# Kernel optimization log

Measured on AMD Instinct MI355X. Metric: run time of the kernel, lower is better.

The kernel has to match this reference:

```python
import jax, jax.numpy as jnp
import numpy as np

H = 28; W = 28; N = H * W
P = N              # padded max persistence pairs per homology dimension
T = 32             # landscape resolution
K1, K2 = 2, 3      # K_max for the two topo layers
M0_1, M0_2 = 0.05, 0.2
LIMS = ((1.0, 28.0), (1.0, 28.0))


def _make_nbrs(h, w, conn8):
    idx = np.arange(h * w).reshape(h, w)
    offs = [(-1, 0), (1, 0), (0, -1), (0, 1)]
    if conn8:
        offs += [(-1, -1), (-1, 1), (1, -1), (1, 1)]
    nbrs = []
    for i in range(h):
        for j in range(w):
            cur = [idx[i + a, j + b] for a, b in offs if 0 <= i + a < h and 0 <= j + b < w]
            nbrs.append(np.asarray(cur, np.int64))
    return nbrs

_NBR4 = _make_nbrs(H, W, False)
_NBR8 = _make_nbrs(H, W, True)


def _h0_pairs(vals, nbrs):
    # 0-dim persistence pairs of a vertex-valued sublevel filtration (union-find, elder rule)
    order = np.argsort(vals, kind="stable")
    pos = np.empty(N, np.int64); pos[order] = np.arange(N)
    parent = np.arange(N); birth = np.arange(N)
    added = np.zeros(N, bool)
    bi = np.zeros(P, np.int32); di = np.zeros(P, np.int32)
    k = 0
    def find(x):
        r = x
        while parent[r] != r: r = parent[r]
        while parent[x] != r: parent[x], x = r, parent[x]
        return r
    for v in order:
        added[v] = True
        for u in nbrs[v]:
            if not added[u]: continue
            ru, rv = find(u), find(v)
            if ru == rv: continue
            if pos[birth[ru]] <= pos[birth[rv]]:
                lb = birth[rv]; parent[rv] = ru
            else:
                lb = birth[ru]; parent[ru] = rv
            if k < P:
                bi[k] = lb; di[k] = v; k += 1
    return bi, di


def _pers_pairs_np(x):
    # x: [M, N] -> (birth_idx, death_idx) each [M, 2, P]; padded pairs point at idx 0 (zero persistence)
    x = np.asarray(x, np.float64)
    M = x.shape[0]
    bi = np.zeros((M, 2, P), np.int32); di = np.zeros((M, 2, P), np.int32)
    for m in range(M):
        b0, d0 = _h0_pairs(x[m], _NBR4)      # H0: sublevel, 4-connectivity
        b1, d1 = _h0_pairs(-x[m], _NBR8)     # H1 by Alexander duality: H0 of superlevel, 8-connectivity
        bi[m, 0], di[m, 0] = b0, d0
        bi[m, 1], di[m, 1] = d1, b1          # H1 birth = vals[d1], death = vals[b1]
    return bi, di


def _grid_d2():
    xs = np.linspace(LIMS[0][0], LIMS[0][1], H)
    ys = np.linspace(LIMS[1][0], LIMS[1][1], W)
    gx, gy = np.meshgrid(xs, ys, indexing="ij")
    pts = np.stack([gx.ravel(), gy.ravel()], 1)              # [N, 2] grid coordinates
    d2 = ((pts[:, None, :] - pts[None, :, :]) ** 2).sum(-1)  # [N, N] squared distances
    si = np.argsort(d2, axis=1, kind="stable")
    return jnp.asarray(si), jnp.asarray(np.take_along_axis(d2, si, 1), jnp.float32)

_SORT_IDX, _D2S = _grid_d2()


def dtm(x_flat, m0):
    # weighted distance-to-measure on the pixel grid, r=2; x_flat: [M, N] positive weights
    bound = m0 * jnp.sum(x_flat, -1, keepdims=True)                        # [M, 1]
    ws = x_flat[:, _SORT_IDX]                                              # [M, N, N] weights in distance order
    cum = jnp.cumsum(ws, -1)
    eff = jnp.minimum(jnp.maximum(bound[..., None] - (cum - ws), 0.0), ws) # effective mass per neighbor
    return jnp.sqrt(jnp.sum(eff * _D2S, -1) / bound)                       # [M, N]


def _landscape(vals, bi, di, start, end, K):
    # persistence landscape lambda_k sampled on T points from (birth, death) critical-vertex indices
    M = vals.shape[0]
    mi = jnp.arange(M)[:, None, None]
    b = vals[mi, bi]; d = vals[mi, di]                                     # [M, 2, P]
    t = jnp.linspace(start, end, T, dtype=vals.dtype)                      # [T]
    tent = jnp.maximum(jnp.minimum(t - b[..., None], d[..., None] - t), 0.0)  # [M, 2, P, T]
    lam, _ = jax.lax.top_k(jnp.swapaxes(tent, -1, -2), K)                  # [M, 2, T, K]
    return jnp.swapaxes(lam, -1, -2).reshape(M, 2 * K * T)                 # [M, dims*K*T]


def pl_features(vals, start, end, K):
    M = vals.shape[0]
    bi, di = jax.pure_callback(
        _pers_pairs_np,
        (jax.ShapeDtypeStruct((M, 2, P), np.int32),
         jax.ShapeDtypeStruct((M, 2, P), np.int32)),
        jax.lax.stop_gradient(vals))
    return _landscape(vals, bi, di, start, end, K)


def setup_inputs():
    key = jax.random.key(0)
    ks = jax.random.split(key, 7)
    B = 64
    return {
        "input": jax.random.uniform(ks[0], (B, 1, H, W), jnp.float32, 1e-3, 1.0),
        "w_g1": 0.1 * jax.random.normal(ks[1], (32, 2 * K1 * T), jnp.float32),
        "b_g1": 0.1 * jax.random.normal(ks[2], (32,), jnp.float32),
        "w_g2": 0.1 * jax.random.normal(ks[3], (32, 2 * K2 * T), jnp.float32),
        "b_g2": 0.1 * jax.random.normal(ks[4], (32,), jnp.float32),
        "w_fc": 0.1 * jax.random.normal(ks[5], (10, 64), jnp.float32),
        "b_fc": 0.1 * jax.random.normal(ks[6], (10,), jnp.float32),
    }


def reference(input, w_g1, b_g1, w_g2, b_g2, w_fc, b_fc):
    x_flat = input.reshape(-1, N)                                        # num_channels = 1
    f1 = dtm(x_flat, M0_1)
    f2 = dtm(x_flat, M0_2)
    x1 = jax.nn.relu(pl_features(f1, 0.0, 7.0, K1) @ w_g1.T + b_g1)      # topo layer 1 (start=0, end=7, K=2)
    x2 = jax.nn.relu(pl_features(f2, 1.0, 8.0, K2) @ w_g2.T + b_g2)      # topo layer 2 (start=1, end=8, K=3)
    return jnp.concatenate([x1, x2], -1) @ w_fc.T + b_fc                 # [B, num_classes]
```

## Files before the change

### kernel.cpp

```cpp
#include <hip/hip_runtime.h>
#include <algorithm>

#define HW 28
#define NPIX 784
#define NIMG 64
#define MAXREC 5504
#define NOFF 3025
#define NOFFP 3072

#define DXPK 41048u
#define DYPK 34949u

namespace {
struct OffTbl {
    unsigned int t[NOFFP];
    OffTbl() {
        struct E { int d2, lin, dx, dy; };
        static E es[NOFF];
        int n = 0;
        for (int dx = -27; dx <= 27; ++dx)
            for (int dy = -27; dy <= 27; ++dy) {
                es[n].d2 = dx * dx + dy * dy;
                es[n].lin = dx * HW + dy;
                es[n].dx = dx; es[n].dy = dy;
                ++n;
            }
        std::sort(es, es + NOFF, [](const E& a, const E& b) {
            return a.d2 != b.d2 ? a.d2 < b.d2 : a.lin < b.lin;
        });
        for (int k2 = 0; k2 < NOFF; ++k2)
            t[k2] = ((unsigned)es[k2].d2 << 16) |
                    ((unsigned)(es[k2].dx + 27) << 8) |
                    (unsigned)(es[k2].dy + 27);
        for (int k2 = NOFF; k2 < NOFFP; ++k2) t[k2] = 0xFFFFFFFFu;
    }
};
OffTbl g_offtbl;
}

__global__ void xt_sums_kernel(const float* __restrict__ x,
                               float* __restrict__ sums,
                               float* __restrict__ xT) {
    int tid = threadIdx.x;
    int m = blockIdx.x;
    const float* xr = x + m * NPIX;
    float acc = 0.f;
    for (int j = tid; j < NPIX; j += 256) {
        float v = xr[j];
        xT[j * NIMG + m] = v;
        acc += v;
    }
    for (int off = 32; off > 0; off >>= 1) acc += __shfl_down(acc, off, 64);
    __shared__ float red[4];
    int lane = tid & 63, w = tid >> 6;
    if (lane == 0) red[w] = acc;
    __syncthreads();
    if (tid == 0) sums[m] = red[0] + red[1] + red[2] + red[3];
}

__global__ void __launch_bounds__(256) sortdtm_kernel(const unsigned int* __restrict__ OTB,
                               const float* __restrict__ xT,
                               const float* __restrict__ sums,
                               float* __restrict__ F) {
    __shared__ unsigned int tpl[NPIX];
    __shared__ int wtot[4];
    int tid = threadIdx.x;
    int i = blockIdx.x;
    int ii = i / HW, ij = i % HW;

    const uint4* o4 = (const uint4*)OTB + tid * 3;
    uint4 qa = o4[0], qb = o4[1], qc = o4[2];
    unsigned int ent[12] = {qa.x, qa.y, qa.z, qa.w,
                            qb.x, qb.y, qb.z, qb.w,
                            qc.x, qc.y, qc.z, qc.w};
    int ct = 0;
    #pragma unroll
    for (int e = 0; e < 12; ++e) {
        int dx = (int)((ent[e] >> 8) & 255u) - 27;
        int dy = (int)(ent[e] & 255u) - 27;
        ct += ((unsigned)(ii + dx) < (unsigned)HW && (unsigned)(ij + dy) < (unsigned)HW) ? 1 : 0;
    }
    int lane = tid & 63, wv = tid >> 6;
    int p = ct;
    for (int off = 1; off < 64; off <<= 1) {
        int t2 = __shfl_up(p, off, 64);
        if (lane >= off) p += t2;
    }
    if (lane == 63) wtot[wv] = p;
    __syncthreads();
    int slot = p - ct;
    for (int w2 = 0; w2 < wv; ++w2) slot += wtot[w2];
    #pragma unroll
    for (int e = 0; e < 12; ++e) {
        int dx = (int)((ent[e] >> 8) & 255u) - 27;
        int dy = (int)(ent[e] & 255u) - 27;
        int ui = ii + dx, uj = ij + dy;
        if ((unsigned)ui < (unsigned)HW && (unsigned)uj < (unsigned)HW) {
            tpl[slot] = (unsigned)(ui * HW + uj) | (ent[e] & 0xFFFF0000u);
            ++slot;
        }
    }
    __syncthreads();

    if (tid < 64) {
        float s = sums[tid];
        float bound1 = 0.05f * s, bound2 = 0.2f * s;
        float cum = 0.f, acc1 = 0.f, acc2 = 0.f;
        for (int t0 = 0; t0 < NPIX; t0 += 8) {
            unsigned int e[8];
            #pragma unroll
            for (int u = 0; u < 8; ++u) e[u] = tpl[t0 + u];
            float w[8];
            #pragma unroll
            for (int u = 0; u < 8; ++u) w[u] = xT[(e[u] & 0xffffu) * NIMG + tid];
            #pragma unroll
            for (int u = 0; u < 8; ++u) {
                float d2 = (float)(e[u] >> 16);
                float ce = cum;
                cum += w[u];
                acc1 += fminf(fmaxf(bound1 - ce, 0.f), w[u]) * d2;
                acc2 += fminf(fmaxf(bound2 - ce, 0.f), w[u]) * d2;
            }
            if (__ballot(cum < bound2) == 0ull) break;
        }
        F[0 * NIMG * NPIX + tid * NPIX + i] = sqrtf(acc1 / bound1);
        F[1 * NIMG * NPIX + tid * NPIX + i] = sqrtf(acc2 / bound2);
    }
}

template<int NN>
__device__ int uf_basin_run(const int* posA, const int* ordA,
                            int* bas, unsigned int* pb, int* comp,
                            int* recs, int* pairsI,
                            int2* mergeLDS, int* shInts, int* wtot16) {
    const int tid = threadIdx.x;
    const int lane = tid & 63, wv = tid >> 6;

    for (int s = tid; s < NPIX; s += 1024) {
        int si = s / HW, sj = s % HW;
        int bestPos = posA[s], best = s;
        #pragma unroll
        for (int o = 0; o < NN; ++o) {
            int dx = ((DXPK >> (2 * o)) & 3) - 1;
            int dy = ((DYPK >> (2 * o)) & 3) - 1;
            int ui = si + dx, uj = sj + dy;
            if ((unsigned)ui < (unsigned)HW && (unsigned)uj < (unsigned)HW) {
                int u = ui * HW + uj;
                int pu = posA[u];
                if (pu < bestPos) { bestPos = pu; best = u; }
            }
        }
        bas[s] = best;
    }
    __syncthreads();

    for (int it = 0; it < 10; ++it) {
        int changed = 0;
        for (int s = tid; s < NPIX; s += 1024) {
            int b = bas[s];
            int bb = bas[b];
            if (bb != b) { bas[s] = bb; changed = 1; }
        }
        if (__syncthreads_count(changed) == 0) break;
    }

    for (int s = tid; s < NPIX; s += 1024)
        pb[s] = ((unsigned)posA[s] << 10) | (unsigned)bas[s];
    __syncthreads();

    int nrec = 0;
    {
        int r = tid;
        int cnt = 0;
        int myr[NN - 1];
        int got[NN - 1];
        #pragma unroll
        for (int t = 0; t < NN - 1; ++t) { got[t] = -1; myr[t] = 0; }
        if (r > 0 && r < NPIX) {
            int v = ordA[r];
            int vi = v / HW, vj = v % HW;
            int pivot = (int)(pb[v] & 1023u);
            #pragma unroll
            for (int o = 0; o < NN; ++o) {
                int dx = ((DXPK >> (2 * o)) & 3) - 1;
                int dy = ((DYPK >> (2 * o)) & 3) - 1;
                int ui = vi + dx, uj = vj + dy;
                if ((unsigned)ui < (unsigned)HW && (unsigned)uj < (unsigned)HW) {
                    int u = ui * HW + uj;
                    unsigned e = pb[u];
                    if ((int)(e >> 10) < r) {
                        int b = (int)(e & 1023u);
                        bool dup = (b == pivot);
                        #pragma unroll
                        for (int t = 0; t < NN - 1; ++t) dup = dup || (got[t] == b);
                        if (!dup) {
                            #pragma unroll
                            for (int t = 0; t < NN - 1; ++t)
                                if (t == cnt) { got[t] = b; myr[t] = (v << 20) | (pivot << 10) | b; }
                            cnt++;
                        }
                    }
                }
            }
        }
        int p = cnt;
        for (int off = 1; off < 64; off <<= 1) {
            int t2 = __shfl_up(p, off, 64);
            if (lane >= off) p += t2;
        }
        if (lane == 63) wtot16[wv] = p;
        __syncthreads();
        int wadd = 0;
        for (int w2 = 0; w2 < wv; ++w2) wadd += wtot16[w2];
        int tot = 0;
        #pragma unroll
        for (int w2 = 0; w2 < 16; ++w2) tot += wtot16[w2];
        int excl = wadd + p - cnt;
        #pragma unroll
        for (int t = 0; t < NN - 1; ++t)
            if (t < cnt) recs[excl + t] = myr[t];
        nrec = tot;
        __syncthreads();
    }

    int k = 0;
    for (int base = 0; base < nrec; base += 64) {
        int nrem = 0;
        if (wv == 0) {
            int idx = base + lane;
            int rec = (idx < nrec) ? recs[idx] : 0;
            int pa = (rec >> 10) & 1023, pbn = rec & 1023;
            int ka = 0, kb = 0;
            if (idx < nrec) { ka = comp[pa]; kb = comp[pbn]; }
            for (;;) {
                unsigned long long d = __ballot(ka != kb);
                if (d == 0ull) break;
                int i = (int)__ffsll((long long)d) - 1;
                int sA = __builtin_amdgcn_readlane(ka, i);
                int sB = __builtin_amdgcn_readlane(kb, i);
                int w = min(sA, sB), l = max(sA, sB);
                int sv = __builtin_amdgcn_readlane(rec, i) >> 20;
                if (lane == 0) {
                    pairsI[k] = (l & 1023) | (sv << 10);
                    mergeLDS[nrem] = make_int2(l, w);
                }
                k++;
                ka = (ka == l) ? w : ka;
                kb = (kb == l) ? w : kb;
                nrem++;
                if (nrem == 63) {
                    for (int s = lane; s < NPIX; s += 64) {
                        int cv = comp[s], c0 = cv;
                        for (int e = 0; e < nrem; ++e) {
                            int2 me = mergeLDS[e];
                            cv = (cv == me.x) ? me.y : cv;
                        }
                        if (cv != c0) comp[s] = cv;
                    }
                    if (idx < nrec) { ka = comp[pa]; kb = comp[pbn]; }
                    nrem = 0;
                }
            }
            if (lane == 0) shInts[0] = nrem;
        }
        __syncthreads();
        int nr = shInts[0];
        if (nr > 0) {
            for (int s = tid; s < NPIX; s += 1024) {
                int cv = comp[s], c0 = cv;
                for (int e = 0; e < nr; ++e) {
                    int2 me = mergeLDS[e];
                    cv = (cv == me.x) ? me.y : cv;
                }
                if (cv != c0) comp[s] = cv;
            }
        }
        __syncthreads();
    }
    if (tid == 0) shInts[1] = k;
    __syncthreads();
    return shInts[1];
}

__global__ void __launch_bounds__(1024) uf_land_kernel(const float* __restrict__ F,
                                                       float* __restrict__ LAM1,
                                                       float* __restrict__ LAM2) {
    __shared__ int posA[NPIX], ordA[NPIX], bas[NPIX], comp[NPIX], pairsI[NPIX];
    __shared__ unsigned int pbArr[NPIX];
    __shared__ alignas(16) unsigned long long key64[NPIX];
    __shared__ float fv[NPIX];
    __shared__ alignas(16) int recs[MAXREC];
    __shared__ int2 mergeLDS[64];
    __shared__ int shInts[2];
    __shared__ int wtot16[16];
    int tid = threadIdx.x;
    int task = blockIdx.x;
    int feat = task >> 7;
    int dir = (task >> 6) & 1;
    int m = task & 63;
    const float* fr = F + feat * NIMG * NPIX + m * NPIX;

    for (int j = tid; j < NPIX; j += 1024) {
        float f = fr[j];
        fv[j] = f;
        unsigned int b = __float_as_uint(f);
        if (dir) b = ~b;
        key64[j] = ((unsigned long long)b << 10) | (unsigned)j;
    }
    __syncthreads();

    if (tid < NPIX) {
        unsigned long long pki = key64[tid];
        int rank = 0;
        const ulonglong2* k2 = (const ulonglong2*)key64;
        for (int c = 0; c < NPIX / 2; ++c) {
            ulonglong2 kv = k2[c];
            rank += (int)(kv.x < pki) + (int)(kv.y < pki);
        }
        posA[tid] = rank;
        ordA[rank] = tid;
    }
    __syncthreads();
    for (int s = tid; s < NPIX; s += 1024) comp[s] = (posA[s] << 10) | s;

    int k;
    if (dir == 0) k = uf_basin_run<4>(posA, ordA, bas, pbArr, comp, recs, pairsI,
                                      mergeLDS, shInts, wtot16);
    else          k = uf_basin_run<8>(posA, ordA, bas, pbArr, comp, recs, pairsI,
                                      mergeLDS, shInts, wtot16);

    float start = (feat == 0) ? 0.f : 1.f;
    float end   = (feat == 0) ? 7.f : 8.f;
    {
        int sub = tid >> 5;
        int t = tid & 31;
        float tv = start + (end - start) * ((float)t / 31.f);
        float v0 = 0.f, v1 = 0.f, v2 = 0.f;
        for (int p = sub; p < k; p += 32) {
            int pi = pairsI[p];
            float fb = fv[pi & 1023], fd = fv[pi >> 10];
            float bb = dir ? fd : fb;
            float dd = dir ? fb : fd;
            float tent = fmaxf(fminf(tv - bb, dd - tv), 0.f);
            if (tent > v0)      { v2 = v1; v1 = v0; v0 = tent; }
            else if (tent > v1) { v2 = v1; v1 = tent; }
            else if (tent > v2) { v2 = tent; }
        }
        float* part = (float*)recs;
        int bse = (sub * 32 + t) * 3;
        part[bse] = v0; part[bse + 1] = v1; part[bse + 2] = v2;
    }
    __syncthreads();
    if (tid < 32) {
        int t = tid;
        const float* part = (const float*)recs;
        float v0 = 0.f, v1 = 0.f, v2 = 0.f;
        for (int s2 = 0; s2 < 32; ++s2) {
            int bse = (s2 * 32 + t) * 3;
            #pragma unroll
            for (int q = 0; q < 3; ++q) {
                float x = part[bse + q];
                if (x > v0)      { v2 = v1; v1 = v0; v0 = x; }
                else if (x > v1) { v2 = v1; v1 = x; }
                else if (x > v2) { v2 = x; }
            }
        }
        if (feat == 0) {
            float* lam = LAM1 + m * 128 + dir * 64;
            lam[0 * 32 + t] = v0;
            lam[1 * 32 + t] = v1;
        } else {
            float* lam = LAM2 + m * 192 + dir * 96;
            lam[0 * 32 + t] = v0;
            lam[1 * 32 + t] = v1;
            lam[2 * 32 + t] = v2;
        }
    }
}

__global__ void mlp_kernel(const float* __restrict__ LAM1, const float* __restrict__ LAM2,
                           const float* __restrict__ w1, const float* __restrict__ b1,
                           const float* __restrict__ w2, const float* __restrict__ b2,
                           const float* __restrict__ wf, const float* __restrict__ bf,
                           float* __restrict__ out) {
    __shared__ float xc[64];
    int m = blockIdx.x;
    int n = threadIdx.x;
    if (n < 32) {
        float acc = b1[n];
        const float* l = LAM1 + m * 128;
        for (int c = 0; c < 128; ++c) acc += w1[n * 128 + c] * l[c];
        xc[n] = fmaxf(acc, 0.f);
    } else {
        int n2 = n - 32;
        float acc = b2[n2];
        const float* l = LAM2 + m * 192;
        for (int c = 0; c < 192; ++c) acc += w2[n2 * 192 + c] * l[c];
        xc[n] = fmaxf(acc, 0.f);
    }
    __syncthreads();
    if (n < 10) {
        float acc = bf[n];
        for (int c = 0; c < 64; ++c) acc += wf[n * 64 + c] * xc[c];
        out[m * 10 + n] = acc;
    }
}

extern "C" void kernel_launch(void* const* d_in, const int* in_sizes, int n_in,
                              void* d_out, int out_size, void* d_ws, size_t ws_size,
                              hipStream_t stream) {
    const float* x  = (const float*)d_in[0];
    const float* w1 = (const float*)d_in[1];
    const float* b1 = (const float*)d_in[2];
    const float* w2 = (const float*)d_in[3];
    const float* b2 = (const float*)d_in[4];
    const float* wf = (const float*)d_in[5];
    const float* bf = (const float*)d_in[6];
    float* out = (float*)d_out;

    char* ws = (char*)d_ws;
    size_t off = 0;
    unsigned int* OTB = (unsigned int*)(ws + off); off += (size_t)NOFFP * 4;
    float* XT   = (float*)(ws + off); off += (size_t)NPIX * NIMG * 4;
    float* SUMS = (float*)(ws + off); off += 256;
    float* F    = (float*)(ws + off); off += (size_t)2 * NIMG * NPIX * 4;
    float* LAM1 = (float*)(ws + off); off += (size_t)NIMG * 128 * 4;
    float* LAM2 = (float*)(ws + off); off += (size_t)NIMG * 192 * 4;

    hipMemcpyAsync(OTB, g_offtbl.t, (size_t)NOFFP * 4, hipMemcpyHostToDevice, stream);
    xt_sums_kernel<<<NIMG, 256, 0, stream>>>(x, SUMS, XT);
    sortdtm_kernel<<<NPIX, 256, 0, stream>>>(OTB, XT, SUMS, F);
    uf_land_kernel<<<256, 1024, 0, stream>>>(F, LAM1, LAM2);
    mlp_kernel<<<NIMG, 64, 0, stream>>>(LAM1, LAM2, w1, b1, w2, b2, wf, bf, out);
}
```

Baseline: 127.8 us.

## Bake offset table into device constant, widen DTM unroll, serialize landscape top-k

The sorted offset table is now built at compile time as a constexpr __device__ constant, which removes the per-call host-to-device memcpy. The DTM accumulation loop is unrolled by 16 instead of 8, giving more independent gathers per early-exit ballot check. The landscape top-3 reduction now runs in a single warp of 32 threads that loops over every pair, replacing the two-level 1024-thread partial reduction and its extra barrier. That trades parallelism in the landscape step for less synchronisation and shared-memory traffic.

```diff
diff --git a/kernel.cpp b/kernel.cpp
--- a/kernel.cpp
+++ b/kernel.cpp
@@ -1,5 +1,4 @@
 #include <hip/hip_runtime.h>
-#include <algorithm>
 
 #define HW 28
 #define NPIX 784
@@ -7,36 +6,51 @@
 #define MAXREC 5504
 #define NOFF 3025
 #define NOFFP 3072
+#define ND2 1459
 
 #define DXPK 41048u
 #define DYPK 34949u
 
-namespace {
-struct OffTbl {
-    unsigned int t[NOFFP];
-    OffTbl() {
-        struct E { int d2, lin, dx, dy; };
-        static E es[NOFF];
-        int n = 0;
-        for (int dx = -27; dx <= 27; ++dx)
-            for (int dy = -27; dy <= 27; ++dy) {
-                es[n].d2 = dx * dx + dy * dy;
-                es[n].lin = dx * HW + dy;
-                es[n].dx = dx; es[n].dy = dy;
-                ++n;
-            }
-        std::sort(es, es + NOFF, [](const E& a, const E& b) {
-            return a.d2 != b.d2 ? a.d2 < b.d2 : a.lin < b.lin;
-        });
-        for (int k2 = 0; k2 < NOFF; ++k2)
-            t[k2] = ((unsigned)es[k2].d2 << 16) |
-                    ((unsigned)(es[k2].dx + 27) << 8) |
-                    (unsigned)(es[k2].dy + 27);
-        for (int k2 = NOFF; k2 < NOFFP; ++k2) t[k2] = 0xFFFFFFFFu;
-    }
-};
-OffTbl g_offtbl;
-}
+struct alignas(16) OffTbl { unsigned int t[NOFFP]; };
+
+static constexpr OffTbl make_offtbl() {
+    OffTbl o{};
+    int cnt[ND2] = {};
+    for (int dx = -27; dx <= 27; ++dx)
+        for (int dy = -27; dy <= 27; ++dy)
+            cnt[dx * dx + dy * dy]++;
+    int pos[ND2] = {};
+    int run = 0;
+    for (int b = 0; b < ND2; ++b) { pos[b] = run; run += cnt[b]; }
+    int lin_[NOFF] = {}, dxs[NOFF] = {}, dys[NOFF] = {};
+    int p2[ND2] = {};
+    for (int b = 0; b < ND2; ++b) p2[b] = pos[b];
+    for (int dx = -27; dx <= 27; ++dx)
+        for (int dy = -27; dy <= 27; ++dy) {
+            int d2 = dx * dx + dy * dy;
+            int s = p2[d2]++;
+            lin_[s] = dx * HW + dy; dxs[s] = dx; dys[s] = dy;
+        }
+    for (int b = 0; b < ND2; ++b) {
+        int s0 = pos[b], s1 = pos[b] + cnt[b];
+        for (int a = s0 + 1; a < s1; ++a) {
+            int L = lin_[a], X = dxs[a], Y = dys[a];
+            int c = a;
+            while (c > s0 && lin_[c - 1] > L) {
+                lin_[c] = lin_[c - 1]; dxs[c] = dxs[c - 1]; dys[c] = dys[c - 1];
+                --c;
+            }
+            lin_[c] = L; dxs[c] = X; dys[c] = Y;
+        }
+    }
+    for (int s = 0; s < NOFF; ++s)
+        o.t[s] = ((unsigned)(dxs[s] * dxs[s] + dys[s] * dys[s]) << 16) |
+                 ((unsigned)(dxs[s] + 27) << 8) | (unsigned)(dys[s] + 27);
+    for (int s = NOFF; s < NOFFP; ++s) o.t[s] = 0xFFFFFFFFu;
+    return o;
+}
+
+__device__ const OffTbl OTBC = make_offtbl();
 
 __global__ void xt_sums_kernel(const float* __restrict__ x,
                                float* __restrict__ sums,
@@ -58,17 +72,16 @@
     if (tid == 0) sums[m] = red[0] + red[1] + red[2] + red[3];
 }
 
-__global__ void __launch_bounds__(256) sortdtm_kernel(const unsigned int* __restrict__ OTB,
-                               const float* __restrict__ xT,
-                               const float* __restrict__ sums,
-                               float* __restrict__ F) {
+__global__ void __launch_bounds__(256) sortdtm_kernel(const float* __restrict__ xT,
+                                                      const float* __restrict__ sums,
+                                                      float* __restrict__ F) {
     __shared__ unsigned int tpl[NPIX];
     __shared__ int wtot[4];
     int tid = threadIdx.x;
     int i = blockIdx.x;
     int ii = i / HW, ij = i % HW;
 
-    const uint4* o4 = (const uint4*)OTB + tid * 3;
+    const uint4* o4 = (const uint4*)OTBC.t + tid * 3;
     uint4 qa = o4[0], qb = o4[1], qc = o4[2];
     unsigned int ent[12] = {qa.x, qa.y, qa.z, qa.w,
                             qb.x, qb.y, qb.z, qb.w,
@@ -106,15 +119,15 @@
         float s = sums[tid];
         float bound1 = 0.05f * s, bound2 = 0.2f * s;
         float cum = 0.f, acc1 = 0.f, acc2 = 0.f;
-        for (int t0 = 0; t0 < NPIX; t0 += 8) {
-            unsigned int e[8];
+        for (int t0 = 0; t0 < NPIX; t0 += 16) {
+            unsigned int e[16];
             #pragma unroll
-            for (int u = 0; u < 8; ++u) e[u] = tpl[t0 + u];
-            float w[8];
+            for (int u = 0; u < 16; ++u) e[u] = tpl[t0 + u];
+            float w[16];
             #pragma unroll
-            for (int u = 0; u < 8; ++u) w[u] = xT[(e[u] & 0xffffu) * NIMG + tid];
+            for (int u = 0; u < 16; ++u) w[u] = xT[(e[u] & 0xffffu) * NIMG + tid];
             #pragma unroll
-            for (int u = 0; u < 8; ++u) {
+            for (int u = 0; u < 16; ++u) {
                 float d2 = (float)(e[u] >> 16);
                 float ce = cum;
                 cum += w[u];
@@ -289,7 +302,7 @@
     __shared__ unsigned int pbArr[NPIX];
     __shared__ alignas(16) unsigned long long key64[NPIX];
     __shared__ float fv[NPIX];
-    __shared__ alignas(16) int recs[MAXREC];
+    __shared__ int recs[MAXREC];
     __shared__ int2 mergeLDS[64];
     __shared__ int shInts[2];
     __shared__ int wtot16[16];
@@ -329,14 +342,13 @@
     else          k = uf_basin_run<8>(posA, ordA, bas, pbArr, comp, recs, pairsI,
                                       mergeLDS, shInts, wtot16);
 
-    float start = (feat == 0) ? 0.f : 1.f;
-    float end   = (feat == 0) ? 7.f : 8.f;
-    {
-        int sub = tid >> 5;
-        int t = tid & 31;
+    if (tid < 32) {
+        int t = tid;
+        float start = (feat == 0) ? 0.f : 1.f;
+        float end   = (feat == 0) ? 7.f : 8.f;
         float tv = start + (end - start) * ((float)t / 31.f);
         float v0 = 0.f, v1 = 0.f, v2 = 0.f;
-        for (int p = sub; p < k; p += 32) {
+        for (int p = 0; p < k; ++p) {
             int pi = pairsI[p];
             float fb = fv[pi & 1023], fd = fv[pi >> 10];
             float bb = dir ? fd : fb;
@@ -345,25 +357,6 @@
             if (tent > v0)      { v2 = v1; v1 = v0; v0 = tent; }
             else if (tent > v1) { v2 = v1; v1 = tent; }
             else if (tent > v2) { v2 = tent; }
-        }
-        float* part = (float*)recs;
-        int bse = (sub * 32 + t) * 3;
-        part[bse] = v0; part[bse + 1] = v1; part[bse + 2] = v2;
-    }
-    __syncthreads();
-    if (tid < 32) {
-        int t = tid;
-        const float* part = (const float*)recs;
-        float v0 = 0.f, v1 = 0.f, v2 = 0.f;
-        for (int s2 = 0; s2 < 32; ++s2) {
-            int bse = (s2 * 32 + t) * 3;
-            #pragma unroll
-            for (int q = 0; q < 3; ++q) {
-                float x = part[bse + q];
-                if (x > v0)      { v2 = v1; v1 = v0; v0 = x; }
-                else if (x > v1) { v2 = v1; v1 = x; }
-                else if (x > v2) { v2 = x; }
-            }
         }
         if (feat == 0) {
             float* lam = LAM1 + m * 128 + dir * 64;
@@ -420,16 +413,14 @@
 
     char* ws = (char*)d_ws;
     size_t off = 0;
-    unsigned int* OTB = (unsigned int*)(ws + off); off += (size_t)NOFFP * 4;
     float* XT   = (float*)(ws + off); off += (size_t)NPIX * NIMG * 4;
     float* SUMS = (float*)(ws + off); off += 256;
     float* F    = (float*)(ws + off); off += (size_t)2 * NIMG * NPIX * 4;
     float* LAM1 = (float*)(ws + off); off += (size_t)NIMG * 128 * 4;
     float* LAM2 = (float*)(ws + off); off += (size_t)NIMG * 192 * 4;
 
-    hipMemcpyAsync(OTB, g_offtbl.t, (size_t)NOFFP * 4, hipMemcpyHostToDevice, stream);
     xt_sums_kernel<<<NIMG, 256, 0, stream>>>(x, SUMS, XT);
-    sortdtm_kernel<<<NPIX, 256, 0, stream>>>(OTB, XT, SUMS, F);
+    sortdtm_kernel<<<NPIX, 256, 0, stream>>>(XT, SUMS, F);
     uf_land_kernel<<<256, 1024, 0, stream>>>(F, LAM1, LAM2);
     mlp_kernel<<<NIMG, 64, 0, stream>>>(LAM1, LAM2, w1, b1, w2, b2, wf, bf, out);
 }
```

Result: faster. 118.7 us, median of 2 (-7.1%).
